# Optimization experiments

Measured on AMD Instinct MI355X. Metric: run time of the kernel, lower is better.

The kernel has to match this reference:

```python
import jax, jax.numpy as jnp
import numpy as np

# FP4 E2M1 lookup: low 3 bits -> magnitude {0,.5,1,1.5,2,3,4,6}, bit 3 -> sign
FP4_LUT = jnp.array([0.0, 0.5, 1.0, 1.5, 2.0, 3.0, 4.0, 6.0,
                     -0.0, -0.5, -1.0, -1.5, -2.0, -3.0, -4.0, -6.0], dtype=jnp.float32)


def _dequant(packed_i32, scales, group_size):
    """packed_i32: [K/8, N] (8 FP4 nibbles per word along K); scales: [K/group_size, N] fp16.
    Returns dense [K, N] float32 weight."""
    p = packed_i32.astype(jnp.uint32)
    shifts = (jnp.arange(8, dtype=jnp.uint32) * jnp.uint32(4))
    nib = ((p[:, None, :] >> shifts[None, :, None]) & jnp.uint32(0xF)).astype(jnp.int32)  # [K/8,8,N]
    K = p.shape[0] * 8
    vals = FP4_LUT[nib.reshape(K, p.shape[1])]  # [K, N] f32
    g = jnp.arange(K) // group_size
    return vals * scales.astype(jnp.float32)[g]


def setup_inputs() -> dict:
    key = jax.random.key(0)
    k1, k2, k3, k4, k5 = jax.random.split(key, 5)
    B, H, I, G = 32, 4096, 2048, 128
    x = (jax.random.normal(k1, (B, H), dtype=jnp.float32) * 0.5).astype(jnp.float16)
    gate_up_packed = jax.random.bits(k2, (H // 8, 2 * I), dtype=jnp.uint32).astype(jnp.int32)
    down_packed = jax.random.bits(k3, (I // 8, H), dtype=jnp.uint32).astype(jnp.int32)
    gate_up_scales = (jax.random.uniform(k4, (H // G, 2 * I), minval=0.005, maxval=0.02)).astype(jnp.float16)
    down_scales = (jax.random.uniform(k5, (I // G, H), minval=0.005, maxval=0.02)).astype(jnp.float16)
    return {"x": x, "gate_up_packed": gate_up_packed, "gate_up_scales": gate_up_scales,
            "down_packed": down_packed, "down_scales": down_scales, "group_size": G}


def reference(x, gate_up_packed, gate_up_scales, down_packed, down_scales, group_size):
    w_gu = _dequant(gate_up_packed, gate_up_scales, group_size)   # [H, 2I]
    h = jnp.einsum('bh,hn->bn', x.astype(jnp.float32), w_gu)      # [B, 2I]
    inter = h.shape[1] // 2
    act = jax.nn.silu(h[:, :inter]) * h[:, inter:]                # SwiGLU
    w_d = _dequant(down_packed, down_scales, group_size)          # [I, H]
    out = jnp.einsum('bi,ih->bh', act, w_d)
    return out.astype(jnp.float16)
```

## Files before the change

kernel.cpp:

```cpp
#include <hip/hip_runtime.h>
#include <cstdint>

typedef float f32x4 __attribute__((ext_vector_type(4)));
typedef __fp16 f16;
typedef f16 f16x2 __attribute__((ext_vector_type(2)));
typedef f16 f16x8 __attribute__((ext_vector_type(8)));

constexpr int Bv = 32;
constexpr int Hv = 4096;
constexpr int Iv = 2048;
constexpr int N1 = 4096;

__device__ __forceinline__ f16x8 dec8h(uint32_t w) {
  uint32_t lo = w & 0x07070707u;
  uint32_t hi = (w >> 4) & 0x07070707u;
  uint32_t e = __builtin_amdgcn_perm(0x46444240u, 0x3E3C3800u, lo)
             | ((w & 0x08080808u) << 4);
  uint32_t o = __builtin_amdgcn_perm(0x46444240u, 0x3E3C3800u, hi)
             | (w & 0x80808080u);
  union { uint32_t u[4]; f16x8 v; } r;
  r.u[0] = __builtin_amdgcn_perm(e, 0u, 0x05000400u);
  r.u[1] = __builtin_amdgcn_perm(e, 0u, 0x07000600u);
  r.u[2] = __builtin_amdgcn_perm(o, 0u, 0x05000400u);
  r.u[3] = __builtin_amdgcn_perm(o, 0u, 0x07000600u);
  return r.v;
}

__device__ __forceinline__ f16x8 packA(const float* p) {
  f32x4 a = *(const f32x4*)p;
  f32x4 b = *(const f32x4*)(p + 4);
  union { f16x2 h[4]; f16x8 v; } r;
  r.h[0] = __builtin_amdgcn_cvt_pkrtz(a[0], a[2]);
  r.h[1] = __builtin_amdgcn_cvt_pkrtz(b[0], b[2]);
  r.h[2] = __builtin_amdgcn_cvt_pkrtz(a[1], a[3]);
  r.h[3] = __builtin_amdgcn_cvt_pkrtz(a[1 + 2], a[3]);
  r.h[2] = __builtin_amdgcn_cvt_pkrtz(a[1], a[3]);
  r.h[3] = __builtin_amdgcn_cvt_pkrtz(b[1], b[3]);
  return r.v;
}

__global__ __launch_bounds__(1024, 4) void k_gus(
    const float* __restrict__ x, const uint32_t* __restrict__ wp,
    const float* __restrict__ sc, f16* __restrict__ act) {
  __shared__ float lds[16 * 512];
  const int b = blockIdx.x;
  const int wid = threadIdx.x >> 6, lane = threadIdx.x & 63;
  const int q = lane >> 4, r = lane & 15;
  const int ncol = (r < 8) ? (b * 8 + r) : (Iv + b * 8 + (r - 8));

  const float* px0 = x + r * Hv + wid * 256 + q * 8;
  const float* px1 = px0 + 16 * Hv;
  const uint32_t* pb = wp + (size_t)(wid * 32 + q) * N1 + ncol;
  const float* ps = sc + (size_t)(wid * 2) * N1 + ncol;

  f32x4 a0g0 = {0,0,0,0}, a1g0 = {0,0,0,0};
  f32x4 a0g1 = {0,0,0,0}, a1g1 = {0,0,0,0};
  #pragma unroll
  for (int st = 0; st < 4; ++st) {
    f16x8 A0 = packA(px0 + st * 32);
    f16x8 A1 = packA(px1 + st * 32);
    f16x8 B  = dec8h(pb[(size_t)(st * 4) * N1]);
    a0g0 = __builtin_amdgcn_mfma_f32_16x16x32_f16(A0, B, a0g0, 0, 0, 0);
    a1g0 = __builtin_amdgcn_mfma_f32_16x16x32_f16(A1, B, a1g0, 0, 0, 0);
  }
  #pragma unroll
  for (int st = 0; st < 4; ++st) {
    f16x8 A0 = packA(px0 + 128 + st * 32);
    f16x8 A1 = packA(px1 + 128 + st * 32);
    f16x8 B  = dec8h(pb[(size_t)(16 + st * 4) * N1]);
    a0g1 = __builtin_amdgcn_mfma_f32_16x16x32_f16(A0, B, a0g1, 0, 0, 0);
    a1g1 = __builtin_amdgcn_mfma_f32_16x16x32_f16(A1, B, a1g1, 0, 0, 0);
  }
  const float s0 = ps[0], s1 = ps[N1];
  float* my = lds + wid * 512;
  #pragma unroll
  for (int j = 0; j < 4; ++j) {
    const int rw = q * 4 + j;
    my[rw * 16 + r]        = s0 * a0g0[j] + s1 * a0g1[j];
    my[(16 + rw) * 16 + r] = s0 * a1g0[j] + s1 * a1g1[j];
  }
  __syncthreads();
  const int i = threadIdx.x;
  if (i < 512) {
    float sum = 0.f;
    #pragma unroll
    for (int w = 0; w < 16; ++w) sum += lds[w * 512 + i];
    const float peer = __shfl_xor(sum, 8, 64);
    const int c = i & 15;
    if (c < 8) {
      const float g = sum, u = peer;
      const float av = g / (1.0f + __expf(-g)) * u;
      const int pos = (c & 1) ? (4 + (c >> 1)) : (c >> 1);
      act[(i >> 4) * Iv + b * 8 + pos] = (f16)av;
    }
  }
}

__global__ __launch_bounds__(1024, 4) void k_down(
    const f16* __restrict__ act, const uint32_t* __restrict__ wp,
    const float* __restrict__ sc, float* __restrict__ out) {
  __shared__ float lds[16 * 512];
  const int n0 = blockIdx.x * 16;
  const int wid = threadIdx.x >> 6, lane = threadIdx.x & 63;
  const int q = lane >> 4, r = lane & 15;
  const int n = n0 + r;

  const int koff = wid * 128 + q * 8;
  const f16* pa0 = act + r * Iv + koff;
  const f16* pa1 = act + (r + 16) * Iv + koff;
  const uint32_t* pb = wp + (size_t)(wid * 16 + q) * Hv + n;

  f32x4 t0 = {0,0,0,0}, t1 = {0,0,0,0};
  #pragma unroll
  for (int st = 0; st < 4; ++st) {
    f16x8 A0 = *(const f16x8*)(pa0 + st * 32);
    f16x8 A1 = *(const f16x8*)(pa1 + st * 32);
    f16x8 B  = dec8h(pb[(size_t)st * 4 * Hv]);
    t0 = __builtin_amdgcn_mfma_f32_16x16x32_f16(A0, B, t0, 0, 0, 0);
    t1 = __builtin_amdgcn_mfma_f32_16x16x32_f16(A1, B, t1, 0, 0, 0);
  }
  const float sv = sc[wid * Hv + n];
  float* my = lds + wid * 512;
  #pragma unroll
  for (int j = 0; j < 4; ++j) {
    const int rw = q * 4 + j;
    my[rw * 16 + r]        = sv * t0[j];
    my[(16 + rw) * 16 + r] = sv * t1[j];
  }
  __syncthreads();
  const int i = threadIdx.x;
  if (i < 512) {
    float sum = 0.f;
    #pragma unroll
    for (int w = 0; w < 16; ++w) sum += lds[w * 512 + i];
    out[(i >> 4) * N1 + n0 + (i & 15)] = sum;
  }
}

extern "C" void kernel_launch(void* const* d_in, const int* in_sizes, int n_in,
                              void* d_out, int out_size, void* d_ws, size_t ws_size,
                              hipStream_t stream) {
  const float*    x   = (const float*)d_in[0];
  const uint32_t* gup = (const uint32_t*)d_in[1];
  const float*    gus = (const float*)d_in[2];
  const uint32_t* dnp = (const uint32_t*)d_in[3];
  const float*    dns = (const float*)d_in[4];

  f16* act = (f16*)d_ws;

  k_gus <<<256, 1024, 0, stream>>>(x, gup, gus, act);
  k_down<<<256, 1024, 0, stream>>>(act, dnp, dns, (float*)d_out);
}
```

Before: 91.33 us.

## Split gate-up kernel by batch half with separate gate and up MFMA tiles

Each gate-up block now handles one half of the batch rows and a 16-column tile, decoding both the gate and the up weight tiles and running separate MFMAs for each. This replaces the previous scheme, where 8 gate and 8 up columns shared one tile and both batch halves reused one decoded B operand. The aim is to fill all 16 MFMA columns with useful output and change the per-block work mix, at the cost of each weight word being loaded and decoded by two blocks. It also removes the redundant duplicate conversions in packA and reworks the LDS reduction and SwiGLU epilogue.

```diff
diff --git a/kernel.cpp b/kernel.cpp
--- a/kernel.cpp
+++ b/kernel.cpp
@@ -33,8 +33,6 @@
   r.h[0] = __builtin_amdgcn_cvt_pkrtz(a[0], a[2]);
   r.h[1] = __builtin_amdgcn_cvt_pkrtz(b[0], b[2]);
   r.h[2] = __builtin_amdgcn_cvt_pkrtz(a[1], a[3]);
-  r.h[3] = __builtin_amdgcn_cvt_pkrtz(a[1 + 2], a[3]);
-  r.h[2] = __builtin_amdgcn_cvt_pkrtz(a[1], a[3]);
   r.h[3] = __builtin_amdgcn_cvt_pkrtz(b[1], b[3]);
   return r.v;
 }
@@ -43,56 +41,58 @@
     const float* __restrict__ x, const uint32_t* __restrict__ wp,
     const float* __restrict__ sc, f16* __restrict__ act) {
   __shared__ float lds[16 * 512];
-  const int b = blockIdx.x;
+  const int mh = blockIdx.x & 1;
+  const int ct = blockIdx.x >> 1;
   const int wid = threadIdx.x >> 6, lane = threadIdx.x & 63;
   const int q = lane >> 4, r = lane & 15;
-  const int ncol = (r < 8) ? (b * 8 + r) : (Iv + b * 8 + (r - 8));
+  const int cg = ct * 16 + r;
 
-  const float* px0 = x + r * Hv + wid * 256 + q * 8;
-  const float* px1 = px0 + 16 * Hv;
-  const uint32_t* pb = wp + (size_t)(wid * 32 + q) * N1 + ncol;
-  const float* ps = sc + (size_t)(wid * 2) * N1 + ncol;
+  const float* px = x + (size_t)(mh * 16 + r) * Hv + wid * 256 + q * 8;
+  const uint32_t* pbA = wp + (size_t)(wid * 32 + q) * N1 + cg;
+  const uint32_t* pbB = pbA + Iv;
+  const float* ps = sc + (size_t)(wid * 2) * N1 + cg;
 
-  f32x4 a0g0 = {0,0,0,0}, a1g0 = {0,0,0,0};
-  f32x4 a0g1 = {0,0,0,0}, a1g1 = {0,0,0,0};
+  f32x4 ga0 = {0,0,0,0}, ua0 = {0,0,0,0};
+  f32x4 ga1 = {0,0,0,0}, ua1 = {0,0,0,0};
   #pragma unroll
   for (int st = 0; st < 4; ++st) {
-    f16x8 A0 = packA(px0 + st * 32);
-    f16x8 A1 = packA(px1 + st * 32);
-    f16x8 B  = dec8h(pb[(size_t)(st * 4) * N1]);
-    a0g0 = __builtin_amdgcn_mfma_f32_16x16x32_f16(A0, B, a0g0, 0, 0, 0);
-    a1g0 = __builtin_amdgcn_mfma_f32_16x16x32_f16(A1, B, a1g0, 0, 0, 0);
+    f16x8 A  = packA(px + st * 32);
+    f16x8 BA = dec8h(pbA[(size_t)(st * 4) * N1]);
+    f16x8 BB = dec8h(pbB[(size_t)(st * 4) * N1]);
+    ga0 = __builtin_amdgcn_mfma_f32_16x16x32_f16(A, BA, ga0, 0, 0, 0);
+    ua0 = __builtin_amdgcn_mfma_f32_16x16x32_f16(A, BB, ua0, 0, 0, 0);
   }
   #pragma unroll
   for (int st = 0; st < 4; ++st) {
-    f16x8 A0 = packA(px0 + 128 + st * 32);
-    f16x8 A1 = packA(px1 + 128 + st * 32);
-    f16x8 B  = dec8h(pb[(size_t)(16 + st * 4) * N1]);
-    a0g1 = __builtin_amdgcn_mfma_f32_16x16x32_f16(A0, B, a0g1, 0, 0, 0);
-    a1g1 = __builtin_amdgcn_mfma_f32_16x16x32_f16(A1, B, a1g1, 0, 0, 0);
+    f16x8 A  = packA(px + 128 + st * 32);
+    f16x8 BA = dec8h(pbA[(size_t)(16 + st * 4) * N1]);
+    f16x8 BB = dec8h(pbB[(size_t)(16 + st * 4) * N1]);
+    ga1 = __builtin_amdgcn_mfma_f32_16x16x32_f16(A, BA, ga1, 0, 0, 0);
+    ua1 = __builtin_amdgcn_mfma_f32_16x16x32_f16(A, BB, ua1, 0, 0, 0);
   }
-  const float s0 = ps[0], s1 = ps[N1];
+  const float sg0 = ps[0],  sg1 = ps[N1];
+  const float su0 = ps[Iv], su1 = ps[N1 + Iv];
   float* my = lds + wid * 512;
   #pragma unroll
   for (int j = 0; j < 4; ++j) {
     const int rw = q * 4 + j;
-    my[rw * 16 + r]        = s0 * a0g0[j] + s1 * a0g1[j];
-    my[(16 + rw) * 16 + r] = s0 * a1g0[j] + s1 * a1g1[j];
+    my[rw * 32 + r]      = sg0 * ga0[j] + sg1 * ga1[j];
+    my[rw * 32 + 16 + r] = su0 * ua0[j] + su1 * ua1[j];
   }
   __syncthreads();
   const int i = threadIdx.x;
-  if (i < 512) {
-    float sum = 0.f;
+  if (i < 256) {
+    const int row = i >> 4, c = i & 15;
+    float g = 0.f, u = 0.f;
     #pragma unroll
-    for (int w = 0; w < 16; ++w) sum += lds[w * 512 + i];
-    const float peer = __shfl_xor(sum, 8, 64);
-    const int c = i & 15;
-    if (c < 8) {
-      const float g = sum, u = peer;
-      const float av = g / (1.0f + __expf(-g)) * u;
-      const int pos = (c & 1) ? (4 + (c >> 1)) : (c >> 1);
-      act[(i >> 4) * Iv + b * 8 + pos] = (f16)av;
+    for (int w = 0; w < 16; ++w) {
+      g += lds[w * 512 + row * 32 + c];
+      u += lds[w * 512 + row * 32 + 16 + c];
     }
+    const float av = g / (1.0f + __expf(-g)) * u;
+    const int d = c & 7;
+    const int pos = (d & 1) ? (4 + (d >> 1)) : (d >> 1);
+    act[(size_t)(mh * 16 + row) * Iv + ct * 16 + (c & 8) + pos] = (f16)av;
   }
 }
 
```

Measured after the change: 85.94 us. 5.9% less time.
